# Optimization experiments

Hardware: AMD Instinct MI355X
Metric: run time of the kernel (lower is better)

The kernel has to match this reference:

```python
import jax, jax.numpy as jnp
import numpy as np

KERNEL = (9, 9, 9)  # box-filter window
KSIZE = KERNEL[0] * KERNEL[1] * KERNEL[2]  # 729
GAMMA = 1.0


def _box_sum(x):
    # x: [B, C, D, H, W] -> channel-sum then 9x9x9 sliding-window sum (SAME pad),
    # exactly matching F.conv3d with an all-ones [1, C, 9,9,9] kernel, pad=4.
    s = jnp.sum(x, axis=1, keepdims=True)  # [B,1,D,H,W]
    return jax.lax.reduce_window(
        s, jnp.asarray(0.0, s.dtype), jax.lax.add,
        window_dimensions=(1, 1) + KERNEL,
        window_strides=(1, 1, 1, 1, 1),
        padding='SAME')


def setup_inputs() -> dict:
    key = jax.random.key(0)
    k1, k2, k3 = jax.random.split(key, 3)
    shape = (2, 1, 160, 160, 160)
    return {
        'input': jax.random.normal(k1, shape, dtype=jnp.float32),
        'target': jax.random.normal(k2, shape, dtype=jnp.float32),
        'flow': jax.random.normal(k3, shape, dtype=jnp.float32),
    }


def reference(input, target, flow):
    # normalize target from (-1, 1) to (0, 1)
    target = (target + 1.0) * 0.5
    w = jax.nn.sigmoid(flow) ** GAMMA  # voxel-wise confidence weight

    T_sum = _box_sum(target)
    I_sum = _box_sum(input)
    TT_sum = _box_sum(target * target)
    II_sum = _box_sum(input * input)
    IT_sum = _box_sum(input * target)

    Ihat = I_sum / KSIZE
    That = T_sum / KSIZE
    cross = IT_sum - Ihat * T_sum - That * I_sum + That * Ihat * KSIZE
    T_var = TT_sum - 2.0 * That * T_sum + That * That * KSIZE
    I_var = II_sum - 2.0 * Ihat * I_sum + Ihat * Ihat * KSIZE

    cc = cross * cross * w / (T_var * I_var + 1e-5)
    return -1.0 * jnp.mean(cc)
```

## Files before the change

### kernel.cpp

```cpp
#include <hip/hip_runtime.h>


constexpr int NB = 2;
constexpr int ND = 160;
constexpr int NH = 160;
constexpr int NW = 160;
constexpr int TH = 16;
constexpr int TW = 16;
constexpr int DCHUNK = 32;
constexpr int NDCH = ND / DCHUNK;
constexpr int NPL = DCHUNK + 8;
constexpr int NIT = NPL + 1;
constexpr int TRS = 20;
constexpr int TFS = 24 * TRS + 8;
constexpr int PRS = 16;
constexpr int PFS = 16 * PRS + 8;
constexpr float INV_K = 1.0f / 729.0f;
constexpr double INV_COUNT = 1.0 / (double(NB) * ND * NH * NW);

__device__ __forceinline__ void gld_lds16(const float* g, float* l)
{
    __builtin_amdgcn_global_load_lds(
        (const __attribute__((address_space(1))) void*)g,
        (__attribute__((address_space(3))) void*)l, 16, 0, 0);
}

__device__ __forceinline__ void dma_plane(const float* __restrict__ in,
                                          const float* __restrict__ tg,
                                          float* __restrict__ inT,
                                          float* __restrict__ tgT,
                                          int b, int dp, int h0, int w0, int tid)
{
    if (tid < 144) {
        int r = tid / 6;
        int q = tid - r * 6;
        int gh = h0 - 4 + r;
        int gw = w0 - 4 + q * 4;
        int wb = (tid >> 6) * 256;
        if (((unsigned)gh < (unsigned)NH) && ((unsigned)gw < (unsigned)NW)) {
            int base = ((b * ND + dp) * NH + gh) * NW + gw;
            gld_lds16(in + base, inT + wb);
            gld_lds16(tg + base, tgT + wb);
        }
    }
}

#define W9SLIDE(EXPR, FI)                                                  \
    {                                                                      \
        float p0 = (EXPR(0)), p1 = (EXPR(1)), p2 = (EXPR(2)),              \
              p3 = (EXPR(3)), p4 = (EXPR(4)), p5 = (EXPR(5)),              \
              p6 = (EXPR(6)), p7 = (EXPR(7)), p8 = (EXPR(8)),              \
              p9 = (EXPR(9)), p10 = (EXPR(10)), p11 = (EXPR(11));          \
        float s = p0 + p1 + p2 + p3 + p4 + p5 + p6 + p7 + p8;              \
        float4 o;                                                          \
        o.x = s; s += p9 - p0;                                             \
        o.y = s; s += p10 - p1;                                            \
        o.z = s; s += p11 - p2;                                            \
        o.w = s;                                                           \
        *reinterpret_cast<float4*>(outp + (FI) * TFS) = o;                 \
    }

__device__ __forceinline__ void step2q(int tid, const float* __restrict__ inT,
                                       const float* __restrict__ tgT,
                                       float* __restrict__ t5)
{
    const int r = tid >> 2, q = tid & 3;
    const float4* ip = reinterpret_cast<const float4*>(inT + r * 24 + 4 * q);
    const float4* tp = reinterpret_cast<const float4*>(tgT + r * 24 + 4 * q);
    const float4 i0 = ip[0], i1 = ip[1], i2 = ip[2];
    const float4 t0 = tp[0], t1 = tp[1], t2 = tp[2];
    const float ia[12] = {i0.x, i0.y, i0.z, i0.w, i1.x, i1.y, i1.z, i1.w,
                          i2.x, i2.y, i2.z, i2.w};
    float ta[12] = {t0.x, t0.y, t0.z, t0.w, t1.x, t1.y, t1.z, t1.w,
                    t2.x, t2.y, t2.z, t2.w};
    #pragma unroll
    for (int j = 0; j < 12; ++j) ta[j] = fmaf(ta[j], 0.5f, 0.5f);
    float* outp = t5 + r * TRS + 4 * q;
    #define E_T(j)  ta[j]
    #define E_I(j)  ia[j]
    #define E_TT(j) (ta[j] * ta[j])
    #define E_II(j) (ia[j] * ia[j])
    #define E_IT(j) (ia[j] * ta[j])
    W9SLIDE(E_T, 0)
    W9SLIDE(E_I, 1)
    W9SLIDE(E_TT, 2)
    W9SLIDE(E_II, 3)
    W9SLIDE(E_IT, 4)
    #undef E_T
    #undef E_I
    #undef E_TT
    #undef E_II
    #undef E_IT
}

__device__ __forceinline__ void hpass(int t, const float* __restrict__ t5,
                                      float* __restrict__ Pb)
{
    const int f = t >> 4;
    const int rem = t & 15;
    const int wq = rem >> 2, hs = rem & 3;
    const float* bp = t5 + f * TFS + hs * 4 * TRS + wq * 4;
    float4 r4[12];
    #pragma unroll
    for (int k = 0; k < 12; ++k)
        r4[k] = *reinterpret_cast<const float4*>(bp + k * TRS);
    float sx = r4[0].x, sy = r4[0].y, sz = r4[0].z, sw = r4[0].w;
    #pragma unroll
    for (int k = 1; k < 9; ++k) {
        sx += r4[k].x; sy += r4[k].y; sz += r4[k].z; sw += r4[k].w;
    }
    float* op = Pb + f * PFS + hs * 4 * PRS + wq * 4;
    *reinterpret_cast<float4*>(op) = make_float4(sx, sy, sz, sw);
    #pragma unroll
    for (int j = 1; j < 4; ++j) {
        sx += r4[8 + j].x - r4[j - 1].x;
        sy += r4[8 + j].y - r4[j - 1].y;
        sz += r4[8 + j].z - r4[j - 1].z;
        sw += r4[8 + j].w - r4[j - 1].w;
        *reinterpret_cast<float4*>(op + j * PRS) = make_float4(sx, sy, sz, sw);
    }
}

__device__ __forceinline__ float cc_value(const float S[5], float flv)
{
    float wgt = 1.0f / (1.0f + __expf(-flv));
    float Ts = S[0], Is = S[1], TTs = S[2], IIs = S[3], ITs = S[4];
    float Ihat = Is * INV_K;
    float That = Ts * INV_K;
    float cross = ITs - Ihat * Ts - That * Is + That * Ihat * 729.0f;
    float T_var = TTs - 2.0f * That * Ts + That * That * 729.0f;
    float I_var = IIs - 2.0f * Ihat * Is + Ihat * Ihat * 729.0f;
    return cross * cross * wgt / (T_var * I_var + 1e-5f);
}

__global__ void __launch_bounds__(256, 4)
cc3d_main(const float* __restrict__ in, const float* __restrict__ tg,
          const float* __restrict__ fl, double* __restrict__ acc_out)
{
    __shared__ __align__(16) float inT[24 * 24];
    __shared__ __align__(16) float tgT[24 * 24];
    __shared__ __align__(16) float tmp5[5 * TFS];
    __shared__ __align__(16) float Pb[5 * PFS];
    __shared__ float red[4];

    const int tid = threadIdx.x;
    const int w0 = blockIdx.x * TW;
    const int h0 = blockIdx.y * TH;
    const int bz = blockIdx.z;
    const int b  = bz / NDCH;
    const int d0 = (bz - b * NDCH) * DCHUNK;
    const int hh = tid >> 4, ww = tid & 15;

    float ring[45];
    #pragma unroll
    for (int i = 0; i < 45; ++i) ring[i] = 0.f;
    float S[5] = {0.f, 0.f, 0.f, 0.f, 0.f};
    float acc = 0.f;
    float flv = 0.f;

    for (int i = tid; i < 576; i += 256) { inT[i] = 0.f; tgT[i] = -1.f; }
    __syncthreads();
    if (d0 - 4 >= 0) dma_plane(in, tg, inT, tgT, b, d0 - 4, h0, w0, tid);

    for (int lb = 0; lb < NIT; lb += 9) {
        #pragma unroll
        for (int li = 0; li < 9; ++li) {
            const int l = lb + li;
            if (l < NIT) {
                if (l >= 1) {
                    const bool vz = ((unsigned)(d0 - 5 + l) < (unsigned)ND);
                    const int slot = (li + 8) % 9;
                    #pragma unroll
                    for (int f = 0; f < 5; ++f) {
                        float pn = vz ? Pb[f * PFS + hh * PRS + ww] : 0.f;
                        S[f] += pn - ring[f * 9 + slot];
                        ring[f * 9 + slot] = pn;
                    }
                    if (l >= 9) acc += cc_value(S, flv);
                }
                __syncthreads();
                const int dpl = d0 - 4 + l;
                const bool vl = (l < NPL) && ((unsigned)dpl < (unsigned)ND);
                if (vl && tid < 96) step2q(tid, inT, tgT, tmp5);
                __syncthreads();
                if (vl && tid >= 176) hpass(tid - 176, tmp5, Pb);
                if (l + 1 < NPL && (unsigned)(dpl + 1) < (unsigned)ND)
                    dma_plane(in, tg, inT, tgT, b, dpl + 1, h0, w0, tid);
                if (l >= 8 && l < 40) {
                    int dout = d0 + l - 8;
                    flv = fl[((b * ND + dout) * NH + (h0 + hh)) * NW + (w0 + ww)];
                }
                __syncthreads();
            }
        }
    }

    #pragma unroll
    for (int off = 32; off > 0; off >>= 1) acc += __shfl_down(acc, off);
    if ((tid & 63) == 0) red[tid >> 6] = acc;
    __syncthreads();
    if (tid == 0) {
        double v = (double)red[0] + (double)red[1] + (double)red[2] + (double)red[3];
        atomicAdd(acc_out, v);
    }
}

__global__ void cc3d_finalize(const double* __restrict__ acc, float* __restrict__ out)
{
    out[0] = (float)(-(acc[0] * INV_COUNT));
}

extern "C" void kernel_launch(void* const* d_in, const int* in_sizes, int n_in,
                              void* d_out, int out_size, void* d_ws, size_t ws_size,
                              hipStream_t stream)
{
    const float* in = (const float*)d_in[0];
    const float* tg = (const float*)d_in[1];
    const float* fl = (const float*)d_in[2];
    float* out = (float*)d_out;
    double* acc = (double*)d_ws;

    hipMemsetAsync(d_ws, 0, sizeof(double), stream);

    dim3 grid(NW / TW, NH / TH, NB * NDCH);
    cc3d_main<<<grid, dim3(256), 0, stream>>>(in, tg, fl, acc);
    cc3d_finalize<<<1, 1, 0, stream>>>(acc, out);
}
```

Baseline: 169.1 us.

## Double-buffer input, partial-sum and flow planes to cut per-plane barriers

Double-buffers the LDS plane tiles, horizontal-pass outputs and a new flow tile. The next plane's DMA and the flow DMA now overlap with the current step. Each plane iteration drops from three full __syncthreads to two custom barriers, one waiting on vmcnt and one only on lgkmcnt. Flow is also staged through LDS instead of a per-thread global load. Out-of-range planes are clamped and loaded instead of skipped, and correctness relies on the vz mask and the tail iterations, which adds redundant DMA traffic and more LDS use per block.

```diff
diff --git a/kernel.cpp b/kernel.cpp
--- a/kernel.cpp
+++ b/kernel.cpp
@@ -25,6 +25,19 @@
         (__attribute__((address_space(3))) void*)l, 16, 0, 0);
 }
 
+__device__ __forceinline__ void bar_vm0()
+{
+    asm volatile("s_waitcnt vmcnt(0) lgkmcnt(0)" ::: "memory");
+    __builtin_amdgcn_s_barrier();
+    __builtin_amdgcn_sched_barrier(0);
+}
+__device__ __forceinline__ void bar_ds()
+{
+    asm volatile("s_waitcnt lgkmcnt(0)" ::: "memory");
+    __builtin_amdgcn_s_barrier();
+    __builtin_amdgcn_sched_barrier(0);
+}
+
 __device__ __forceinline__ void dma_plane(const float* __restrict__ in,
                                           const float* __restrict__ tg,
                                           float* __restrict__ inT,
@@ -42,6 +55,18 @@
             gld_lds16(in + base, inT + wb);
             gld_lds16(tg + base, tgT + wb);
         }
+    }
+}
+
+__device__ __forceinline__ void dma_flow(const float* __restrict__ fl,
+                                         float* __restrict__ flT,
+                                         int b, int dout, int h0, int w0, int tid)
+{
+    if (tid < 64) {
+        int gh = h0 + (tid >> 2);
+        int gw = w0 + ((tid & 3) << 2);
+        int base = ((b * ND + dout) * NH + gh) * NW + gw;
+        gld_lds16(fl + base, flT);
     }
 }
 
@@ -94,7 +119,7 @@
 }
 
 __device__ __forceinline__ void hpass(int t, const float* __restrict__ t5,
-                                      float* __restrict__ Pb)
+                                      float* __restrict__ Pbuf)
 {
     const int f = t >> 4;
     const int rem = t & 15;
@@ -109,7 +134,7 @@
     for (int k = 1; k < 9; ++k) {
         sx += r4[k].x; sy += r4[k].y; sz += r4[k].z; sw += r4[k].w;
     }
-    float* op = Pb + f * PFS + hs * 4 * PRS + wq * 4;
+    float* op = Pbuf + f * PFS + hs * 4 * PRS + wq * 4;
     *reinterpret_cast<float4*>(op) = make_float4(sx, sy, sz, sw);
     #pragma unroll
     for (int j = 1; j < 4; ++j) {
@@ -137,10 +162,11 @@
 cc3d_main(const float* __restrict__ in, const float* __restrict__ tg,
           const float* __restrict__ fl, double* __restrict__ acc_out)
 {
-    __shared__ __align__(16) float inT[24 * 24];
-    __shared__ __align__(16) float tgT[24 * 24];
+    __shared__ __align__(16) float inT[2][576];
+    __shared__ __align__(16) float tgT[2][576];
     __shared__ __align__(16) float tmp5[5 * TFS];
-    __shared__ __align__(16) float Pb[5 * PFS];
+    __shared__ __align__(16) float Pb[2][5 * PFS];
+    __shared__ __align__(16) float flT[2][256];
     __shared__ float red[4];
 
     const int tid = threadIdx.x;
@@ -156,41 +182,50 @@
     for (int i = 0; i < 45; ++i) ring[i] = 0.f;
     float S[5] = {0.f, 0.f, 0.f, 0.f, 0.f};
     float acc = 0.f;
-    float flv = 0.f;
-
-    for (int i = tid; i < 576; i += 256) { inT[i] = 0.f; tgT[i] = -1.f; }
+
+    {
+        float* ifl = &inT[0][0];
+        float* tfl = &tgT[0][0];
+        for (int i = tid; i < 1152; i += 256) { ifl[i] = 0.f; tfl[i] = -1.f; }
+    }
     __syncthreads();
-    if (d0 - 4 >= 0) dma_plane(in, tg, inT, tgT, b, d0 - 4, h0, w0, tid);
+    dma_plane(in, tg, inT[0], tgT[0], b, max(d0 - 4, 0), h0, w0, tid);
 
     for (int lb = 0; lb < NIT; lb += 9) {
         #pragma unroll
         for (int li = 0; li < 9; ++li) {
             const int l = lb + li;
             if (l < NIT) {
+                bar_vm0();
+                {
+                    int dpn = d0 + l - 3;
+                    dpn = min(max(dpn, 0), ND - 1);
+                    dma_plane(in, tg, inT[(l + 1) & 1], tgT[(l + 1) & 1],
+                              b, dpn, h0, w0, tid);
+                }
+                {
+                    int dout = d0 + l - 8;
+                    dout = min(max(dout, 0), ND - 1);
+                    dma_flow(fl, flT[l & 1], b, dout, h0, w0, tid);
+                }
+                if (tid < 96) step2q(tid, inT[l & 1], tgT[l & 1], tmp5);
+                bar_ds();
+                if (tid >= 176) hpass(tid - 176, tmp5, Pb[l & 1]);
                 if (l >= 1) {
-                    const bool vz = ((unsigned)(d0 - 5 + l) < (unsigned)ND);
+                    const bool vz = ((unsigned)(d0 + l - 5) < (unsigned)ND);
                     const int slot = (li + 8) % 9;
+                    const float* pb = Pb[(l - 1) & 1];
                     #pragma unroll
                     for (int f = 0; f < 5; ++f) {
-                        float pn = vz ? Pb[f * PFS + hh * PRS + ww] : 0.f;
+                        float pn = vz ? pb[f * PFS + hh * PRS + ww] : 0.f;
                         S[f] += pn - ring[f * 9 + slot];
                         ring[f * 9 + slot] = pn;
                     }
-                    if (l >= 9) acc += cc_value(S, flv);
+                    if (l >= 9) {
+                        float flv = flT[(l - 1) & 1][tid];
+                        acc += cc_value(S, flv);
+                    }
                 }
-                __syncthreads();
-                const int dpl = d0 - 4 + l;
-                const bool vl = (l < NPL) && ((unsigned)dpl < (unsigned)ND);
-                if (vl && tid < 96) step2q(tid, inT, tgT, tmp5);
-                __syncthreads();
-                if (vl && tid >= 176) hpass(tid - 176, tmp5, Pb);
-                if (l + 1 < NPL && (unsigned)(dpl + 1) < (unsigned)ND)
-                    dma_plane(in, tg, inT, tgT, b, dpl + 1, h0, w0, tid);
-                if (l >= 8 && l < 40) {
-                    int dout = d0 + l - 8;
-                    flv = fl[((b * ND + dout) * NH + (h0 + hh)) * NW + (w0 + ww)];
-                }
-                __syncthreads();
             }
         }
     }
```

New measurement: 177.3 us. 1.05x slower.
